# Kernel optimization log

Measured on AMD Instinct MI355X. Metric: run time of the kernel, lower is better.

## Reference

```python
import jax, jax.numpy as jnp
import numpy as np

B, T, D, H = 1, 2048, 1024, 16
HS = D // H  # 64
FF = 4 * D   # 4096
EPS = 1e-6


def rmsnorm(x, w):
    xf = x.astype(jnp.float32)
    n = xf * jax.lax.rsqrt(jnp.mean(xf * xf, axis=-1, keepdims=True) + EPS)
    return n.astype(x.dtype) * w


def setup_inputs() -> dict:
    key = jax.random.key(0)
    ks = jax.random.split(key, 9)
    s = 0.02
    return {
        "x": jax.random.normal(ks[0], (B, T, D), jnp.float32),
        "Wq": jax.random.normal(ks[1], (H, D, HS), jnp.float32) * s,
        "Wk": jax.random.normal(ks[2], (H, D, HS), jnp.float32) * s,
        "Wv": jax.random.normal(ks[3], (H, D, HS), jnp.float32) * s,
        "Wproj": jax.random.normal(ks[4], (H * HS, D), jnp.float32) * s,
        "bproj": jnp.zeros((D,), jnp.float32),
        "W1": jax.random.normal(ks[5], (D, FF), jnp.float32) * s,
        "W2": jax.random.normal(ks[6], (FF, D), jnp.float32) * s,
        "g1": jnp.ones((D,), jnp.float32),
        "g2": jnp.ones((D,), jnp.float32),
    }


def reference(x, Wq, Wk, Wv, Wproj, bproj, W1, W2, g1, g2):
    # --- self attention on RMSNorm(x) ---
    xn = rmsnorm(x, g1)                                   # [B,T,D]
    q = jnp.einsum('btd,hds->bhts', xn, Wq)               # [B,H,T,hs]
    k = jnp.einsum('btd,hds->bhts', xn, Wk)
    v = jnp.einsum('btd,hds->bhts', xn, Wv)
    scale = HS ** -0.5
    wei = jnp.einsum('bhts,bhus->bhtu', q, k) * scale     # [B,H,T,T]
    causal = jnp.tril(jnp.ones((T, T), bool))
    wei = jnp.where(causal, wei, -jnp.inf)
    wei = jax.nn.softmax(wei, axis=-1)
    attn = jnp.einsum('bhtu,bhus->bhts', wei, v)          # [B,H,T,hs]
    attn = attn.transpose(0, 2, 1, 3).reshape(B, T, H * HS)
    sa = attn @ Wproj + bproj                             # [B,T,D]
    x = x + sa
    # --- SiLU FFN on RMSNorm(x) ---
    xn2 = rmsnorm(x, g2)
    h = jax.nn.silu(xn2 @ W1)                             # [B,T,4D]
    x = x + h @ W2
    return x
```

## Files before the change

### kernel.cpp

```cpp
#include <hip/hip_runtime.h>

typedef unsigned short u16;
typedef unsigned int u32;
typedef __attribute__((ext_vector_type(4))) float f32x4;
typedef __attribute__((ext_vector_type(8))) __bf16 bf16x8;

#define T_SEQ 2048
#define DMODEL 1024
#define NHEAD 16
#define HEADS 64
#define FFDIM 4096
#define MNQ 2097152l

__device__ __forceinline__ u16 f2bf(float f) {
  u32 u = __builtin_bit_cast(u32, f);
  u = u + 0x7FFFu + ((u >> 16) & 1u);
  return (u16)(u >> 16);
}

__device__ __forceinline__ void gload_lds16(const u16* g, u16* l) {
  __builtin_amdgcn_global_load_lds(
      (const __attribute__((address_space(1))) u32*)g,
      (__attribute__((address_space(3))) u32*)l, 16, 0, 0);
}

__global__ __launch_bounds__(256) void transpose_qkv_k(
    const float* __restrict__ Wq, const float* __restrict__ Wk,
    const float* __restrict__ Wv, u16* __restrict__ out) {
  __shared__ u16 tile[64 * 66];
  int wsel = blockIdx.z >> 4, h = blockIdx.z & 15;
  const float* inp = (wsel == 0 ? Wq : (wsel == 1 ? Wk : Wv)) + (long)h * 65536;
  u16* outp = out + (long)wsel * 1048576 + (long)h * 65536;
  int r0 = blockIdx.x * 64;
  int tid = threadIdx.x;
#pragma unroll
  for (int p = 0; p < 16; ++p) {
    int idx = p * 256 + tid;
    int r = idx >> 6, c = idx & 63;
    tile[c * 66 + r] = f2bf(inp[(long)(r0 + r) * 64 + c]);
  }
  __syncthreads();
#pragma unroll
  for (int p = 0; p < 16; ++p) {
    int idx = p * 256 + tid;
    int c = idx >> 6, r = idx & 63;
    outp[(long)c * 1024 + r0 + r] = tile[c * 66 + r];
  }
}

__global__ __launch_bounds__(256) void transpose_w_k(
    const float* __restrict__ Wproj, const float* __restrict__ W1,
    const float* __restrict__ W2, u16* __restrict__ WprojT,
    u16* __restrict__ W1T, u16* __restrict__ W2T) {
  __shared__ u16 tile[64 * 66];
  int bid = blockIdx.x;
  const float* in;
  u16* out;
  int ldin, ldout, r0, c0;
  if (bid < 256) {
    in = Wproj; out = WprojT; ldin = 1024; ldout = 1024;
    r0 = (bid >> 4) * 64; c0 = (bid & 15) * 64;
  } else if (bid < 1280) {
    int b = bid - 256;
    in = W1; out = W1T; ldin = 4096; ldout = 1024;
    r0 = (b & 15) * 64; c0 = (b >> 4) * 64;
  } else {
    int b = bid - 1280;
    in = W2; out = W2T; ldin = 1024; ldout = 4096;
    r0 = (b >> 4) * 64; c0 = (b & 15) * 64;
  }
  int tid = threadIdx.x;
#pragma unroll
  for (int p = 0; p < 16; ++p) {
    int idx = p * 256 + tid;
    int r = idx >> 6, c = idx & 63;
    tile[c * 66 + r] = f2bf(in[(long)(r0 + r) * ldin + c0 + c]);
  }
  __syncthreads();
#pragma unroll
  for (int p = 0; p < 16; ++p) {
    int idx = p * 256 + tid;
    int c = idx >> 6, r = idx & 63;
    out[(long)(c0 + c) * ldout + r0 + r] = tile[c * 66 + r];
  }
}

__global__ __launch_bounds__(256) void rmsnorm_k(const float* __restrict__ x,
                                                 const float* __restrict__ g,
                                                 u16* __restrict__ out) {
  int row = blockIdx.x;
  int tid = threadIdx.x;
  const float4* xr = (const float4*)(x + (long)row * DMODEL);
  float4 v = xr[tid];
  float ss = v.x * v.x + v.y * v.y + v.z * v.z + v.w * v.w;
#pragma unroll
  for (int off = 32; off >= 1; off >>= 1) ss += __shfl_xor(ss, off, 64);
  __shared__ float wsum[4];
  if ((tid & 63) == 0) wsum[tid >> 6] = ss;
  __syncthreads();
  float tot = wsum[0] + wsum[1] + wsum[2] + wsum[3];
  float rms = rsqrtf(tot * (1.0f / DMODEL) + 1e-6f);
  float4 gv = ((const float4*)g)[tid];
  ushort4 o4 = make_ushort4(f2bf(v.x * rms * gv.x), f2bf(v.y * rms * gv.y),
                            f2bf(v.z * rms * gv.z), f2bf(v.w * rms * gv.w));
  ((ushort4*)(out + (long)row * DMODEL))[tid] = o4;
}

__global__ __launch_bounds__(256) void proj_rms_k(
    const float* __restrict__ p, const float* __restrict__ bias,
    const float* __restrict__ resid, const float* __restrict__ g,
    float* __restrict__ x1, u16* __restrict__ xn2) {
  int row = blockIdx.x;
  int tid = threadIdx.x;
  long i = (long)row * DMODEL + tid * 4;
  float4 a = *(const float4*)(p + i);
  float4 b = *(const float4*)(p + MNQ + i);
  float4 r = *(const float4*)(resid + i);
  float4 bi = *(const float4*)(bias + tid * 4);
  float4 v;
  v.x = a.x + b.x + r.x + bi.x;
  v.y = a.y + b.y + r.y + bi.y;
  v.z = a.z + b.z + r.z + bi.z;
  v.w = a.w + b.w + r.w + bi.w;
  *(float4*)(x1 + i) = v;
  float ss = v.x * v.x + v.y * v.y + v.z * v.z + v.w * v.w;
#pragma unroll
  for (int off = 32; off >= 1; off >>= 1) ss += __shfl_xor(ss, off, 64);
  __shared__ float wsum[4];
  if ((tid & 63) == 0) wsum[tid >> 6] = ss;
  __syncthreads();
  float tot = wsum[0] + wsum[1] + wsum[2] + wsum[3];
  float rms = rsqrtf(tot * (1.0f / DMODEL) + 1e-6f);
  float4 gv = ((const float4*)g)[tid];
  ushort4 o4 = make_ushort4(f2bf(v.x * rms * gv.x), f2bf(v.y * rms * gv.y),
                            f2bf(v.z * rms * gv.z), f2bf(v.w * rms * gv.w));
  ((ushort4*)(xn2 + (long)row * DMODEL))[tid] = o4;
}

template <int EPI>
__global__ __launch_bounds__(256) void gemm_bt_k(
    const u16* __restrict__ A, const u16* __restrict__ Bt, int N, int K, int kc,
    u16* __restrict__ out16, u16* __restrict__ vt,
    float* __restrict__ p0, float* __restrict__ p1) {
  __shared__ __align__(16) u16 As[128 * 32];
  __shared__ __align__(16) u16 Bs[128 * 32];
  int tid = threadIdx.x;
  int w = tid >> 6, lane = tid & 63;
  int quad = lane >> 4, l15 = lane & 15;
  int m0 = blockIdx.x * 128, n0 = blockIdx.y * 128;
  int kz = blockIdx.z;
  int wr = w >> 1, wc = w & 1;

  f32x4 acc[4][4] = {};

  int srow = w * 32 + (lane >> 2);
  int kch = (lane & 3) * 8;
  const u16* Ag = A + (long)(m0 + srow) * K + kch;
  const u16* Bg = Bt + (long)(n0 + srow) * K + kch;
  u16* AsW = As + w * 1024;
  u16* BsW = Bs + w * 1024;

  int kbeg = kz * kc, kend = kbeg + kc;
  for (int kb = kbeg; kb < kend; kb += 32) {
    gload_lds16(Ag + kb, AsW);
    gload_lds16(Ag + kb + 16 * K, AsW + 512);
    gload_lds16(Bg + kb, BsW);
    gload_lds16(Bg + kb + 16 * K, BsW + 512);
    __syncthreads();
    bf16x8 af[4], bfr[4];
#pragma unroll
    for (int mt = 0; mt < 4; ++mt)
      af[mt] = *(const bf16x8*)(As + (wr * 64 + mt * 16 + l15) * 32 + quad * 8);
#pragma unroll
    for (int nt = 0; nt < 4; ++nt)
      bfr[nt] = *(const bf16x8*)(Bs + (wc * 64 + nt * 16 + l15) * 32 + quad * 8);
#pragma unroll
    for (int mt = 0; mt < 4; ++mt)
#pragma unroll
      for (int nt = 0; nt < 4; ++nt)
        acc[mt][nt] = __builtin_amdgcn_mfma_f32_16x16x32_bf16(
            af[mt], bfr[nt], acc[mt][nt], 0, 0, 0);
    __syncthreads();
  }

  bool vblock = (EPI == 0) && (vt != nullptr) && (n0 >= 2048);
  float* pb = nullptr;
  if (EPI == 4) pb = (kz < 2 ? p0 : p1) + (long)(kz & 1) * MNQ;
#pragma unroll
  for (int mt = 0; mt < 4; ++mt)
#pragma unroll
    for (int nt = 0; nt < 4; ++nt) {
      int col = n0 + wc * 64 + nt * 16 + l15;
      if (EPI == 0 && vblock) {
        int s = col - 2048;
        int row0 = m0 + wr * 64 + mt * 16 + quad * 4;
        ushort4 pk = make_ushort4(f2bf(acc[mt][nt][0]), f2bf(acc[mt][nt][1]),
                                  f2bf(acc[mt][nt][2]), f2bf(acc[mt][nt][3]));
        *(ushort4*)(vt + (long)s * 2048 + row0) = pk;
        continue;
      }
#pragma unroll
      for (int r = 0; r < 4; ++r) {
        int row = m0 + wr * 64 + mt * 16 + quad * 4 + r;
        long idx = (long)row * N + col;
        float v = acc[mt][nt][r];
        if (EPI == 0) {
          out16[idx] = f2bf(v);
        } else if (EPI == 2) {
          out16[idx] = f2bf(v / (1.0f + __expf(-v)));
        } else if (EPI == 4) {
          pb[idx] = v;
        }
      }
    }
}

__global__ __launch_bounds__(256) void reduce_ffn2_k(
    const float* __restrict__ p0, const float* __restrict__ p1,
    const float* __restrict__ resid, float* __restrict__ out) {
  long i = ((long)blockIdx.x * 256 + threadIdx.x) * 4;
  float4 a = *(const float4*)(p0 + i);
  float4 b = *(const float4*)(p0 + MNQ + i);
  float4 c = *(const float4*)(p1 + i);
  float4 d = *(const float4*)(p1 + MNQ + i);
  float4 r = *(const float4*)(resid + i);
  float4 o;
  o.x = a.x + b.x + c.x + d.x + r.x;
  o.y = a.y + b.y + c.y + d.y + r.y;
  o.z = a.z + b.z + c.z + d.z + r.z;
  o.w = a.w + b.w + c.w + d.w + r.w;
  *(float4*)(out + i) = o;
}

#define LSTR 72
__global__ __launch_bounds__(256) void attn_part_k(const u16* __restrict__ QKV,
                                                   const u16* __restrict__ Vt,
                                                   u16* __restrict__ Opart,
                                                   float* __restrict__ lpart) {
  __shared__ __align__(16) u16 Qs[64 * LSTR];
  __shared__ __align__(16) u16 Ks[64 * LSTR];
  __shared__ __align__(16) u16 Vs[64 * LSTR];

  int tid = threadIdx.x;
  int w = tid >> 6, lane = tid & 63;
  int quad = lane >> 4, l15 = lane & 15;
  int h = blockIdx.y;

  int p = blockIdx.x;
  int bx = 0, acc0 = 0;
  while (true) {
    int n = (bx >> 3) + 1;
    if (p < acc0 + n) break;
    acc0 += n;
    ++bx;
  }
  int c = p - acc0;
  int t0 = bx * 64;
  int jstart = c * 8;
  int jend = min(jstart + 8, bx + 1);

#pragma unroll
  for (int pp = 0; pp < 2; ++pp) {
    int idx = pp * 256 + tid;
    int row = idx >> 3, cc = idx & 7;
    *(uint4*)(Qs + row * LSTR + cc * 8) =
        *(const uint4*)(QKV + (long)(t0 + row) * 3072 + h * 64 + cc * 8);
  }
  __syncthreads();
  bf16x8 aq[2];
#pragma unroll
  for (int ks = 0; ks < 2; ++ks)
    aq[ks] = *(const bf16x8*)(Qs + (w * 16 + l15) * LSTR + ks * 32 + quad * 8);

  f32x4 oacc[4] = {};
  float lsum[4] = {0.f, 0.f, 0.f, 0.f};

  u16* PsW = Qs + w * (16 * LSTR);

  for (int j = jstart; j < jend; ++j) {
    __syncthreads();
#pragma unroll
    for (int pp = 0; pp < 2; ++pp) {
      int idx = pp * 256 + tid;
      int row = idx >> 3, cc = idx & 7;
      *(uint4*)(Ks + row * LSTR + cc * 8) =
          *(const uint4*)(QKV + (long)(j * 64 + row) * 3072 + 1024 + h * 64 + cc * 8);
      *(uint4*)(Vs + row * LSTR + cc * 8) =
          *(const uint4*)(Vt + (long)h * (64 * 2048) + (long)row * 2048 + j * 64 + cc * 8);
    }
    __syncthreads();

    f32x4 sacc[4] = {};
#pragma unroll
    for (int ks = 0; ks < 2; ++ks)
#pragma unroll
      for (int nt = 0; nt < 4; ++nt) {
        bf16x8 bk = *(const bf16x8*)(Ks + (nt * 16 + l15) * LSTR + ks * 32 + quad * 8);
        sacc[nt] = __builtin_amdgcn_mfma_f32_16x16x32_bf16(aq[ks], bk, sacc[nt], 0, 0, 0);
      }

    bool boundary = (j == bx);
#pragma unroll
    for (int nt = 0; nt < 4; ++nt)
#pragma unroll
      for (int r = 0; r < 4; ++r) {
        float pv = exp2f(sacc[nt][r] * 0.18033688f);
        if (boundary) {
          int u = j * 64 + nt * 16 + l15;
          int q = t0 + w * 16 + quad * 4 + r;
          if (u > q) pv = 0.f;
        }
        lsum[r] += pv;
        PsW[(quad * 4 + r) * LSTR + nt * 16 + l15] = f2bf(pv);
      }
    asm volatile("s_waitcnt lgkmcnt(0)" ::: "memory");
#pragma unroll
    for (int ks = 0; ks < 2; ++ks) {
      bf16x8 pf = *(const bf16x8*)(PsW + l15 * LSTR + ks * 32 + quad * 8);
#pragma unroll
      for (int ct = 0; ct < 4; ++ct) {
        bf16x8 vf = *(const bf16x8*)(Vs + (ct * 16 + l15) * LSTR + ks * 32 + quad * 8);
        oacc[ct] = __builtin_amdgcn_mfma_f32_16x16x32_bf16(pf, vf, oacc[ct], 0, 0, 0);
      }
    }
  }

#pragma unroll
  for (int off = 8; off >= 1; off >>= 1)
#pragma unroll
    for (int r = 0; r < 4; ++r) lsum[r] += __shfl_xor(lsum[r], off, 64);

  long slot = (long)p * 16 + h;
  float inv[4];
#pragma unroll
  for (int r = 0; r < 4; ++r) inv[r] = 1.0f / lsum[r];
  u16* Ob = Opart + slot * 4096;
#pragma unroll
  for (int ct = 0; ct < 4; ++ct)
#pragma unroll
    for (int r = 0; r < 4; ++r)
      Ob[(w * 16 + quad * 4 + r) * 64 + ct * 16 + l15] = f2bf(oacc[ct][r] * inv[r]);
  if (l15 == 0) {
    float* lp = lpart + slot * 64;
#pragma unroll
    for (int r = 0; r < 4; ++r) lp[w * 16 + quad * 4 + r] = lsum[r];
  }
}

__global__ __launch_bounds__(256) void attn_combine_k(
    const u16* __restrict__ Opart, const float* __restrict__ lpart,
    u16* __restrict__ out) {
  int bx = blockIdx.x, h = blockIdx.y;
  int g = bx >> 3;
  int p0 = 4 * g * (g + 1) + (bx - 8 * g) * (g + 1);
  int nc = g + 1;
  int tid = threadIdx.x;
  int row = tid >> 2, c4 = (tid & 3) * 16;

  float lv[4];
  float wsum = 0.f;
  for (int cidx = 0; cidx < nc; ++cidx) {
    long slot = (long)(p0 + cidx) * 16 + h;
    lv[cidx] = lpart[slot * 64 + row];
    wsum += lv[cidx];
  }
  float rinv = 1.0f / wsum;

  float o[16];
#pragma unroll
  for (int i = 0; i < 16; ++i) o[i] = 0.f;
  for (int cidx = 0; cidx < nc; ++cidx) {
    float wc = lv[cidx] * rinv;
    const u16* Ob = Opart + ((long)(p0 + cidx) * 16 + h) * 4096 + row * 64 + c4;
    bf16x8 a = *(const bf16x8*)Ob;
    bf16x8 b = *(const bf16x8*)(Ob + 8);
#pragma unroll
    for (int i = 0; i < 8; ++i) {
      o[i] += wc * (float)a[i];
      o[8 + i] += wc * (float)b[i];
    }
  }
  u16 ob[16];
#pragma unroll
  for (int i = 0; i < 16; ++i) ob[i] = f2bf(o[i]);
  u16* op = out + (long)(bx * 64 + row) * 1024 + h * 64 + c4;
  *(uint4*)op = *(uint4*)ob;
  *(uint4*)(op + 8) = *(uint4*)(ob + 8);
}

extern "C" void kernel_launch(void* const* d_in, const int* in_sizes, int n_in,
                              void* d_out, int out_size, void* d_ws, size_t ws_size,
                              hipStream_t stream) {
  const float* x     = (const float*)d_in[0];
  const float* Wq    = (const float*)d_in[1];
  const float* Wk    = (const float*)d_in[2];
  const float* Wv    = (const float*)d_in[3];
  const float* Wproj = (const float*)d_in[4];
  const float* bproj = (const float*)d_in[5];
  const float* W1    = (const float*)d_in[6];
  const float* W2    = (const float*)d_in[7];
  const float* g1    = (const float*)d_in[8];
  const float* g2    = (const float*)d_in[9];

  char* ws = (char*)d_ws;
  u16* QKVwT  = (u16*)(ws);
  u16* WprojT = (u16*)(ws + (6ul << 20));
  u16* W1T    = (u16*)(ws + (8ul << 20));
  u16* W2T    = (u16*)(ws + (16ul << 20));
  u16* xn1    = (u16*)(ws + (24ul << 20));
  u16* QKVb   = (u16*)(ws + (28ul << 20));
  u16* VtB    = (u16*)(ws + (40ul << 20));
  u16* attn   = (u16*)(ws + (44ul << 20));
  float* x1   = (float*)(ws + (48ul << 20));
  u16* xn2    = (u16*)(ws + (56ul << 20));
  u16* hbuf   = (u16*)(ws + (60ul << 20));
  u16* Opart    = (u16*)(ws + (48ul << 20));
  float* lpart  = (float*)(ws + (58ul << 20));
  float* projpart = (float*)(ws + (28ul << 20));
  float* ffn2pA = (float*)(ws + (28ul << 20));
  float* ffn2pB = (float*)(ws);
  if (ws_size < (76ul << 20)) return;

  dim3 blk(256);

  transpose_qkv_k<<<dim3(16, 1, 48), blk, 0, stream>>>(Wq, Wk, Wv, QKVwT);
  transpose_w_k<<<dim3(2304), blk, 0, stream>>>(Wproj, W1, W2, WprojT, W1T, W2T);

  rmsnorm_k<<<dim3(2048), blk, 0, stream>>>(x, g1, xn1);
  gemm_bt_k<0><<<dim3(16, 24, 1), blk, 0, stream>>>(
      xn1, QKVwT, 3072, 1024, 1024, QKVb, VtB, nullptr, nullptr);
  attn_part_k<<<dim3(80, 16), blk, 0, stream>>>(QKVb, VtB, Opart, lpart);
  attn_combine_k<<<dim3(32, 16), blk, 0, stream>>>(Opart, lpart, attn);
  gemm_bt_k<4><<<dim3(16, 8, 2), blk, 0, stream>>>(
      attn, WprojT, 1024, 1024, 512, nullptr, nullptr, projpart, nullptr);
  proj_rms_k<<<dim3(2048), blk, 0, stream>>>(projpart, bproj, x, g2, x1, xn2);
  gemm_bt_k<2><<<dim3(16, 32, 1), blk, 0, stream>>>(
      xn2, W1T, 4096, 1024, 1024, hbuf, nullptr, nullptr, nullptr);
  gemm_bt_k<4><<<dim3(16, 8, 4), blk, 0, stream>>>(
      hbuf, W2T, 1024, 4096, 1024, nullptr, nullptr, ffn2pA, ffn2pB);
  reduce_ffn2_k<<<dim3(2048), blk, 0, stream>>>(ffn2pA, ffn2pB, x1, (float*)d_out);
}
```

Baseline: 278.4 us.

## Double-buffer GEMM LDS via registers, merge transposes, split-K proj to four

The GEMM main loop drops direct global-to-LDS loads and uses register-staged double buffering. The next K-slice is loaded into registers while MFMAs run on the current LDS buffer, then written to the other buffer, leaving one barrier per iteration instead of two. The two weight-transpose kernels are merged into one launch. The attention output projection goes from split-K 2 to split-K 4, and proj_rms_k now sums four partials. This raises LDS use and register pressure and adds partial-buffer traffic for the projection.

```diff
diff --git a/kernel.cpp b/kernel.cpp
--- a/kernel.cpp
+++ b/kernel.cpp
@@ -18,54 +18,35 @@
   return (u16)(u >> 16);
 }
 
-__device__ __forceinline__ void gload_lds16(const u16* g, u16* l) {
-  __builtin_amdgcn_global_load_lds(
-      (const __attribute__((address_space(1))) u32*)g,
-      (__attribute__((address_space(3))) u32*)l, 16, 0, 0);
-}
-
-__global__ __launch_bounds__(256) void transpose_qkv_k(
+__global__ __launch_bounds__(256) void transpose_all_k(
     const float* __restrict__ Wq, const float* __restrict__ Wk,
-    const float* __restrict__ Wv, u16* __restrict__ out) {
-  __shared__ u16 tile[64 * 66];
-  int wsel = blockIdx.z >> 4, h = blockIdx.z & 15;
-  const float* inp = (wsel == 0 ? Wq : (wsel == 1 ? Wk : Wv)) + (long)h * 65536;
-  u16* outp = out + (long)wsel * 1048576 + (long)h * 65536;
-  int r0 = blockIdx.x * 64;
-  int tid = threadIdx.x;
-#pragma unroll
-  for (int p = 0; p < 16; ++p) {
-    int idx = p * 256 + tid;
-    int r = idx >> 6, c = idx & 63;
-    tile[c * 66 + r] = f2bf(inp[(long)(r0 + r) * 64 + c]);
-  }
-  __syncthreads();
-#pragma unroll
-  for (int p = 0; p < 16; ++p) {
-    int idx = p * 256 + tid;
-    int c = idx >> 6, r = idx & 63;
-    outp[(long)c * 1024 + r0 + r] = tile[c * 66 + r];
-  }
-}
-
-__global__ __launch_bounds__(256) void transpose_w_k(
-    const float* __restrict__ Wproj, const float* __restrict__ W1,
-    const float* __restrict__ W2, u16* __restrict__ WprojT,
+    const float* __restrict__ Wv, const float* __restrict__ Wproj,
+    const float* __restrict__ W1, const float* __restrict__ W2,
+    u16* __restrict__ QKVwT, u16* __restrict__ WprojT,
     u16* __restrict__ W1T, u16* __restrict__ W2T) {
   __shared__ u16 tile[64 * 66];
   int bid = blockIdx.x;
   const float* in;
   u16* out;
-  int ldin, ldout, r0, c0;
-  if (bid < 256) {
+  long ldin, ldout;
+  int r0, c0;
+  if (bid < 768) {
+    int z = bid >> 4, xi = bid & 15;
+    int wsel = z >> 4, h = z & 15;
+    in = (wsel == 0 ? Wq : (wsel == 1 ? Wk : Wv)) + (long)h * 65536;
+    out = QKVwT + (long)wsel * 1048576 + (long)h * 65536;
+    ldin = 64; ldout = 1024;
+    r0 = xi * 64; c0 = 0;
+  } else if (bid < 1024) {
+    int b = bid - 768;
     in = Wproj; out = WprojT; ldin = 1024; ldout = 1024;
-    r0 = (bid >> 4) * 64; c0 = (bid & 15) * 64;
-  } else if (bid < 1280) {
-    int b = bid - 256;
+    r0 = (b >> 4) * 64; c0 = (b & 15) * 64;
+  } else if (bid < 2048) {
+    int b = bid - 1024;
     in = W1; out = W1T; ldin = 4096; ldout = 1024;
     r0 = (b & 15) * 64; c0 = (b >> 4) * 64;
   } else {
-    int b = bid - 1280;
+    int b = bid - 2048;
     in = W2; out = W2T; ldin = 1024; ldout = 4096;
     r0 = (b >> 4) * 64; c0 = (b & 15) * 64;
   }
@@ -107,21 +88,24 @@
 }
 
 __global__ __launch_bounds__(256) void proj_rms_k(
-    const float* __restrict__ p, const float* __restrict__ bias,
-    const float* __restrict__ resid, const float* __restrict__ g,
-    float* __restrict__ x1, u16* __restrict__ xn2) {
+    const float* __restrict__ p0, const float* __restrict__ p1,
+    const float* __restrict__ bias, const float* __restrict__ resid,
+    const float* __restrict__ g, float* __restrict__ x1,
+    u16* __restrict__ xn2) {
   int row = blockIdx.x;
   int tid = threadIdx.x;
   long i = (long)row * DMODEL + tid * 4;
-  float4 a = *(const float4*)(p + i);
-  float4 b = *(const float4*)(p + MNQ + i);
+  float4 a = *(const float4*)(p0 + i);
+  float4 b = *(const float4*)(p0 + MNQ + i);
+  float4 c = *(const float4*)(p1 + i);
+  float4 d = *(const float4*)(p1 + MNQ + i);
   float4 r = *(const float4*)(resid + i);
   float4 bi = *(const float4*)(bias + tid * 4);
   float4 v;
-  v.x = a.x + b.x + r.x + bi.x;
-  v.y = a.y + b.y + r.y + bi.y;
-  v.z = a.z + b.z + r.z + bi.z;
-  v.w = a.w + b.w + r.w + bi.w;
+  v.x = a.x + b.x + c.x + d.x + r.x + bi.x;
+  v.y = a.y + b.y + c.y + d.y + r.y + bi.y;
+  v.z = a.z + b.z + c.z + d.z + r.z + bi.z;
+  v.w = a.w + b.w + c.w + d.w + r.w + bi.w;
   *(float4*)(x1 + i) = v;
   float ss = v.x * v.x + v.y * v.y + v.z * v.z + v.w * v.w;
 #pragma unroll
@@ -142,8 +126,8 @@
     const u16* __restrict__ A, const u16* __restrict__ Bt, int N, int K, int kc,
     u16* __restrict__ out16, u16* __restrict__ vt,
     float* __restrict__ p0, float* __restrict__ p1) {
-  __shared__ __align__(16) u16 As[128 * 32];
-  __shared__ __align__(16) u16 Bs[128 * 32];
+  __shared__ __align__(16) u16 As[2][128 * 32];
+  __shared__ __align__(16) u16 Bs[2][128 * 32];
   int tid = threadIdx.x;
   int w = tid >> 6, lane = tid & 63;
   int quad = lane >> 4, l15 = lane & 15;
@@ -153,34 +137,57 @@
 
   f32x4 acc[4][4] = {};
 
-  int srow = w * 32 + (lane >> 2);
-  int kch = (lane & 3) * 8;
-  const u16* Ag = A + (long)(m0 + srow) * K + kch;
-  const u16* Bg = Bt + (long)(n0 + srow) * K + kch;
-  u16* AsW = As + w * 1024;
-  u16* BsW = Bs + w * 1024;
+  int srow = tid >> 2;
+  int sch = (tid & 3) * 8;
+  const u16* Ag = A + (long)(m0 + srow) * K + sch;
+  const u16* Ag2 = Ag + (long)64 * K;
+  const u16* Bg = Bt + (long)(n0 + srow) * K + sch;
+  const u16* Bg2 = Bg + (long)64 * K;
+  int wof = srow * 32 + sch;
 
   int kbeg = kz * kc, kend = kbeg + kc;
+
+  uint4 ra0 = *(const uint4*)(Ag + kbeg);
+  uint4 ra1 = *(const uint4*)(Ag2 + kbeg);
+  uint4 rb0 = *(const uint4*)(Bg + kbeg);
+  uint4 rb1 = *(const uint4*)(Bg2 + kbeg);
+  *(uint4*)(As[0] + wof) = ra0;
+  *(uint4*)(As[0] + 64 * 32 + wof) = ra1;
+  *(uint4*)(Bs[0] + wof) = rb0;
+  *(uint4*)(Bs[0] + 64 * 32 + wof) = rb1;
+  __syncthreads();
+
+  int buf = 0;
   for (int kb = kbeg; kb < kend; kb += 32) {
-    gload_lds16(Ag + kb, AsW);
-    gload_lds16(Ag + kb + 16 * K, AsW + 512);
-    gload_lds16(Bg + kb, BsW);
-    gload_lds16(Bg + kb + 16 * K, BsW + 512);
-    __syncthreads();
+    bool more = (kb + 32 < kend);
+    if (more) {
+      ra0 = *(const uint4*)(Ag + kb + 32);
+      ra1 = *(const uint4*)(Ag2 + kb + 32);
+      rb0 = *(const uint4*)(Bg + kb + 32);
+      rb1 = *(const uint4*)(Bg2 + kb + 32);
+    }
     bf16x8 af[4], bfr[4];
 #pragma unroll
     for (int mt = 0; mt < 4; ++mt)
-      af[mt] = *(const bf16x8*)(As + (wr * 64 + mt * 16 + l15) * 32 + quad * 8);
+      af[mt] = *(const bf16x8*)(As[buf] + (wr * 64 + mt * 16 + l15) * 32 + quad * 8);
 #pragma unroll
     for (int nt = 0; nt < 4; ++nt)
-      bfr[nt] = *(const bf16x8*)(Bs + (wc * 64 + nt * 16 + l15) * 32 + quad * 8);
+      bfr[nt] = *(const bf16x8*)(Bs[buf] + (wc * 64 + nt * 16 + l15) * 32 + quad * 8);
 #pragma unroll
     for (int mt = 0; mt < 4; ++mt)
 #pragma unroll
       for (int nt = 0; nt < 4; ++nt)
         acc[mt][nt] = __builtin_amdgcn_mfma_f32_16x16x32_bf16(
             af[mt], bfr[nt], acc[mt][nt], 0, 0, 0);
-    __syncthreads();
+    if (more) {
+      int nb = buf ^ 1;
+      *(uint4*)(As[nb] + wof) = ra0;
+      *(uint4*)(As[nb] + 64 * 32 + wof) = ra1;
+      *(uint4*)(Bs[nb] + wof) = rb0;
+      *(uint4*)(Bs[nb] + 64 * 32 + wof) = rb1;
+      __syncthreads();
+    }
+    buf ^= 1;
   }
 
   bool vblock = (EPI == 0) && (vt != nullptr) && (n0 >= 2048);
@@ -416,24 +423,25 @@
   u16* hbuf   = (u16*)(ws + (60ul << 20));
   u16* Opart    = (u16*)(ws + (48ul << 20));
   float* lpart  = (float*)(ws + (58ul << 20));
-  float* projpart = (float*)(ws + (28ul << 20));
+  float* projp0 = (float*)(ws + (28ul << 20));
+  float* projp1 = (float*)(ws + (60ul << 20));
   float* ffn2pA = (float*)(ws + (28ul << 20));
   float* ffn2pB = (float*)(ws);
   if (ws_size < (76ul << 20)) return;
 
   dim3 blk(256);
 
-  transpose_qkv_k<<<dim3(16, 1, 48), blk, 0, stream>>>(Wq, Wk, Wv, QKVwT);
-  transpose_w_k<<<dim3(2304), blk, 0, stream>>>(Wproj, W1, W2, WprojT, W1T, W2T);
+  transpose_all_k<<<dim3(3072), blk, 0, stream>>>(
+      Wq, Wk, Wv, Wproj, W1, W2, QKVwT, WprojT, W1T, W2T);
 
   rmsnorm_k<<<dim3(2048), blk, 0, stream>>>(x, g1, xn1);
   gemm_bt_k<0><<<dim3(16, 24, 1), blk, 0, stream>>>(
       xn1, QKVwT, 3072, 1024, 1024, QKVb, VtB, nullptr, nullptr);
   attn_part_k<<<dim3(80, 16), blk, 0, stream>>>(QKVb, VtB, Opart, lpart);
   attn_combine_k<<<dim3(32, 16), blk, 0, stream>>>(Opart, lpart, attn);
-  gemm_bt_k<4><<<dim3(16, 8, 2), blk, 0, stream>>>(
-      attn, WprojT, 1024, 1024, 512, nullptr, nullptr, projpart, nullptr);
-  proj_rms_k<<<dim3(2048), blk, 0, stream>>>(projpart, bproj, x, g2, x1, xn2);
+  gemm_bt_k<4><<<dim3(16, 8, 4), blk, 0, stream>>>(
+      attn, WprojT, 1024, 1024, 256, nullptr, nullptr, projp0, projp1);
+  proj_rms_k<<<dim3(2048), blk, 0, stream>>>(projp0, projp1, bproj, x, g2, x1, xn2);
   gemm_bt_k<2><<<dim3(16, 32, 1), blk, 0, stream>>>(
       xn2, W1T, 4096, 1024, 1024, hbuf, nullptr, nullptr, nullptr);
   gemm_bt_k<4><<<dim3(16, 8, 4), blk, 0, stream>>>(
```

Result: faster. 272.5 us (-2.1%).
